# Performance work log

Measured on AMD Instinct MI355X. Metric: run time of the kernel, lower is better.

Reference implementation:

```python
import jax, jax.numpy as jnp
import numpy as np

N_HEADS = 8  # from init_kwargs


def setup_inputs() -> dict:
    key = jax.random.key(0)
    k1, k2, k3 = jax.random.split(key, 3)
    N, Dv, Dk, H, W = 8, 256, 256, 128, 128
    V = jax.random.normal(k1, (N, Dv, H, W), dtype=jnp.float32)
    K = jax.random.normal(k2, (N, Dk, H, W), dtype=jnp.float32)
    Q = jax.random.normal(k3, (N, Dk, H, W), dtype=jnp.float32)
    return {"V": V, "K": K, "Q": Q, "ksize": 5, "dilation": 3}


def _infusion(V, K, Q, ksize, dilation, n_heads):
    # Local dilated-window attention, faithful to the torch im2col version
    # (zero padding => padded taps contribute raw score 0, exp(0)=1 in softmax),
    # but computed shift-by-shift so the (C*k*k, L) unfolded tensors are never
    # materialized.
    N, Dv, H, W = V.shape
    Dk = K.shape[1]
    hd = Dk // n_heads
    vhd = Dv // n_heads
    pad = (ksize // 2) * dilation
    Kp = jnp.pad(K, ((0, 0), (0, 0), (pad, pad), (pad, pad)))
    Vp = jnp.pad(V, ((0, 0), (0, 0), (pad, pad), (pad, pad)))
    Qh = Q.reshape(N, n_heads, hd, H, W)  # channel-major head split, as torch .view

    # scores for each of the ksize*ksize dilated taps: (N, nh, H, W) each
    scores = []
    for fi in range(ksize):
        for fj in range(ksize):
            Ks = Kp[:, :, fi * dilation:fi * dilation + H,
                    fj * dilation:fj * dilation + W].reshape(N, n_heads, hd, H, W)
            scores.append(jnp.einsum('nhdxy,nhdxy->nhxy', Ks, Qh))
    # (N, nh, P, H, W), softmax over window taps P (no 1/sqrt(d) scaling, as in torch)
    att = jax.nn.softmax(jnp.stack(scores, axis=2), axis=2)

    out = jnp.zeros((N, n_heads, vhd, H, W), dtype=V.dtype)
    p = 0
    for fi in range(ksize):
        for fj in range(ksize):
            Vs = Vp[:, :, fi * dilation:fi * dilation + H,
                    fj * dilation:fj * dilation + W].reshape(N, n_heads, vhd, H, W)
            out = out + Vs * att[:, :, p][:, :, None]
            p += 1
    return out.reshape(N, Dv, H, W)


def reference(V, K, Q, ksize, dilation):
    return _infusion(V, K, Q, int(ksize), int(dilation), N_HEADS)
```

## Files before the change

### kernel.cpp

```cpp
#include <hip/hip_runtime.h>


#define Hh 128
#define Ww 128
#define HD 32
#define TAPS 25
#define LROWS 20
#define LSTR 142
#define CHW (LROWS * LSTR)
#define BUFW (2 * CHW)

__global__ __launch_bounds__(256, 2) void infusion_kernel(
    const float* __restrict__ Vt,
    const float* __restrict__ Kt,
    const float* __restrict__ Qt,
    float* __restrict__ Ot)
{
    __shared__ float lbuf[2][BUFW];

    const int tid = threadIdx.x;
    const int tx  = tid & 31;
    const int ty  = tid >> 5;
    const int Rb  = blockIdx.x * 8;
    const int row = Rb + ty;
    const int nh  = blockIdx.y;
    const int xs  = tx << 2;

    const size_t plane = (size_t)Hh * Ww;
    const size_t cbase = (size_t)nh * HD * plane;
    const int qoff = row * Ww + xs;

    bool sgv[3]; int sgo[3]; int sgl[3];
#pragma unroll
    for (int k = 0; k < 3; ++k) {
        const int q  = tid + (k << 8);
        const int lr = q >> 5, xc = q & 31;
        const int r  = Rb + lr - 6;
        const bool ok = (q < 640) && (r >= 0) && (r < Hh);
        sgv[k] = ok;
        sgo[k] = ok ? (r * Ww + (xc << 2)) : 0;
        sgl[k] = (lr < LROWS ? lr : 0) * LSTR + 8 + (xc << 2);
    }

    for (int i = tid; i < 2 * BUFW; i += 256) (&lbuf[0][0])[i] = 0.f;

    float4 stg[6];

    auto loadg = [&](const float* Base, int g) {
        const float* p0 = Base + (size_t)g * plane;
        const float* p1 = p0 + plane;
        stg[0] = *(const float4*)(p0 + sgo[0]);
        stg[1] = *(const float4*)(p0 + sgo[1]);
        stg[2] = *(const float4*)(p0 + sgo[2]);
        stg[3] = *(const float4*)(p1 + sgo[0]);
        stg[4] = *(const float4*)(p1 + sgo[1]);
        stg[5] = *(const float4*)(p1 + sgo[2]);
    };
    auto writeg = [&](int bi) {
#pragma unroll
        for (int cc = 0; cc < 2; ++cc)
#pragma unroll
            for (int k = 0; k < 3; ++k)
                if (sgv[k]) {
                    float* p = &lbuf[bi][cc * CHW + sgl[k]];
                    const float4 v = stg[cc * 3 + k];
                    *(float2*)(p)     = make_float2(v.x, v.y);
                    *(float2*)(p + 2) = make_float2(v.z, v.w);
                }
    };

    float s[4][TAPS];
#pragma unroll
    for (int a = 0; a < 4; ++a)
#pragma unroll
        for (int p = 0; p < TAPS; ++p) s[a][p] = 0.f;

    {
        const float* Kb = Kt + cbase;
        const float* Qb = Qt + cbase;
        float4 qc0 = *(const float4*)(Qb + qoff);
        float4 qc1 = *(const float4*)(Qb + plane + qoff);
        float4 qn0 = qc0, qn1 = qc1;
        loadg(Kb, 0);
        __syncthreads();
        writeg(0);
        loadg(Kb, 2);
        __syncthreads();
#pragma unroll 1
        for (int it = 0; it < 16; ++it) {
            if (it < 15) writeg((it + 1) & 1);
            if (it < 14) loadg(Kb, 2 * it + 4);
            if (it < 15) {
                qn0 = *(const float4*)(Qb + (size_t)(2 * it + 2) * plane + qoff);
                qn1 = *(const float4*)(Qb + (size_t)(2 * it + 3) * plane + qoff);
            }
            const float* lb = &lbuf[it & 1][0];
#pragma unroll
            for (int cc = 0; cc < 2; ++cc) {
                const float4 q = cc ? qc1 : qc0;
#pragma unroll
                for (int fy = 0; fy < 5; ++fy) {
                    const float2* vr =
                        (const float2*)(lb + cc * CHW + (ty + 3 * fy) * LSTR + xs + 2);
                    const float2 w0 = vr[0], w1 = vr[1], w2 = vr[2], w3 = vr[3];
                    const float2 w4 = vr[4], w5 = vr[5], w6 = vr[6], w7 = vr[7];
                    const float v[16] = { w0.x, w0.y, w1.x, w1.y,
                                          w2.x, w2.y, w3.x, w3.y,
                                          w4.x, w4.y, w5.x, w5.y,
                                          w6.x, w6.y, w7.x, w7.y };
#pragma unroll
                    for (int fx = 0; fx < 5; ++fx) {
                        const int p = fy * 5 + fx;
                        s[0][p] = fmaf(v[0 + 3 * fx], q.x, s[0][p]);
                        s[1][p] = fmaf(v[1 + 3 * fx], q.y, s[1][p]);
                        s[2][p] = fmaf(v[2 + 3 * fx], q.z, s[2][p]);
                        s[3][p] = fmaf(v[3 + 3 * fx], q.w, s[3][p]);
                    }
                }
            }
            __syncthreads();
            if (it < 15) { qc0 = qn0; qc1 = qn1; }
        }
    }

    const float* Vb = Vt + cbase;
    float*       Ob = Ot + cbase;
    loadg(Vb, 0);

#pragma unroll
    for (int a = 0; a < 4; ++a) {
        float m = s[a][0];
#pragma unroll
        for (int p = 1; p < TAPS; ++p) m = fmaxf(m, s[a][p]);
        float sum = 0.f;
#pragma unroll
        for (int p = 0; p < TAPS; ++p) { float e = __expf(s[a][p] - m); s[a][p] = e; sum += e; }
        const float rs = 1.0f / sum;
#pragma unroll
        for (int p = 0; p < TAPS; ++p) s[a][p] *= rs;
    }

    {
        writeg(0);
        loadg(Vb, 2);
        __syncthreads();
#pragma unroll 1
        for (int it = 0; it < 16; ++it) {
            if (it < 15) writeg((it + 1) & 1);
            if (it < 14) loadg(Vb, 2 * it + 4);
            const float* lb = &lbuf[it & 1][0];
#pragma unroll
            for (int cc = 0; cc < 2; ++cc) {
                float a0 = 0.f, a1 = 0.f, a2 = 0.f, a3 = 0.f;
#pragma unroll
                for (int fy = 0; fy < 5; ++fy) {
                    const float2* vr =
                        (const float2*)(lb + cc * CHW + (ty + 3 * fy) * LSTR + xs + 2);
                    const float2 w0 = vr[0], w1 = vr[1], w2 = vr[2], w3 = vr[3];
                    const float2 w4 = vr[4], w5 = vr[5], w6 = vr[6], w7 = vr[7];
                    const float v[16] = { w0.x, w0.y, w1.x, w1.y,
                                          w2.x, w2.y, w3.x, w3.y,
                                          w4.x, w4.y, w5.x, w5.y,
                                          w6.x, w6.y, w7.x, w7.y };
#pragma unroll
                    for (int fx = 0; fx < 5; ++fx) {
                        const int p = fy * 5 + fx;
                        a0 = fmaf(v[0 + 3 * fx], s[0][p], a0);
                        a1 = fmaf(v[1 + 3 * fx], s[1][p], a1);
                        a2 = fmaf(v[2 + 3 * fx], s[2][p], a2);
                        a3 = fmaf(v[3 + 3 * fx], s[3][p], a3);
                    }
                }
                *(float4*)(Ob + (size_t)(2 * it + cc) * plane + qoff) =
                    make_float4(a0, a1, a2, a3);
            }
            __syncthreads();
        }
    }
}

extern "C" void kernel_launch(void* const* d_in, const int* in_sizes, int n_in,
                              void* d_out, int out_size, void* d_ws, size_t ws_size,
                              hipStream_t stream) {
    const float* V = (const float*)d_in[0];
    const float* K = (const float*)d_in[1];
    const float* Q = (const float*)d_in[2];
    float* O = (float*)d_out;

    const int N = in_sizes[0] / (256 * Hh * Ww);
    dim3 grid(Hh / 8, N * 8);
    dim3 block(256);
    infusion_kernel<<<grid, block, 0, stream>>>(V, K, Q, O);
}
```

Before: 442.0 us.

## Remap threads to 2 pixels each over 4-row tiles to cut registers

Each thread now computes 2 adjacent pixels instead of 4, and a block covers 4 output rows instead of 8. This halves the per-thread score arrays (50 instead of 100 floats) to ease register pressure. The cost is a larger halo fraction: 16 staged rows for 4 output rows, so K and V are loaded from global memory more times per output. Other changes: shared-memory staging now uses aligned float4 stores, and the trailing barrier after the final iteration is dropped.

Measured after the change: 674.9 us. 1.53x slower.

```diff
diff --git a/kernel.cpp b/kernel.cpp
--- a/kernel.cpp
+++ b/kernel.cpp
@@ -5,10 +5,14 @@
 #define Ww 128
 #define HD 32
 #define TAPS 25
-#define LROWS 20
-#define LSTR 142
+#define TROWS 4
+#define LROWS 16
+#define LSTR 144
 #define CHW (LROWS * LSTR)
-#define BUFW (2 * CHW)
+#define PERW (2 * CHW)
+
+typedef float4 f4;
+typedef float2 f2;
 
 __global__ __launch_bounds__(256, 2) void infusion_kernel(
     const float* __restrict__ Vt,
@@ -16,72 +20,65 @@
     const float* __restrict__ Qt,
     float* __restrict__ Ot)
 {
-    __shared__ float lbuf[2][BUFW];
+    __shared__ alignas(16) float lbuf[2][PERW];
 
     const int tid = threadIdx.x;
-    const int tx  = tid & 31;
-    const int ty  = tid >> 5;
-    const int Rb  = blockIdx.x * 8;
+    const int tx  = tid & 63;
+    const int ty  = tid >> 6;
+    const int Rb  = blockIdx.x * TROWS;
     const int row = Rb + ty;
     const int nh  = blockIdx.y;
-    const int xs  = tx << 2;
+    const int x0  = tx << 1;
 
     const size_t plane = (size_t)Hh * Ww;
     const size_t cbase = (size_t)nh * HD * plane;
-    const int qoff = row * Ww + xs;
+    const int qoff = row * Ww + x0;
 
-    bool sgv[3]; int sgo[3]; int sgl[3];
+    bool sgv[2]; int sgo[2]; float* wp[2];
 #pragma unroll
-    for (int k = 0; k < 3; ++k) {
+    for (int k = 0; k < 2; ++k) {
         const int q  = tid + (k << 8);
         const int lr = q >> 5, xc = q & 31;
         const int r  = Rb + lr - 6;
-        const bool ok = (q < 640) && (r >= 0) && (r < Hh);
+        const bool ok = (r >= 0) && (r < Hh);
         sgv[k] = ok;
         sgo[k] = ok ? (r * Ww + (xc << 2)) : 0;
-        sgl[k] = (lr < LROWS ? lr : 0) * LSTR + 8 + (xc << 2);
+        wp[k]  = &lbuf[0][0] + lr * LSTR + 8 + (xc << 2);
     }
 
-    for (int i = tid; i < 2 * BUFW; i += 256) (&lbuf[0][0])[i] = 0.f;
+    for (int i = tid; i < 2 * PERW; i += 256) (&lbuf[0][0])[i] = 0.f;
 
-    float4 stg[6];
+    const float* Kb = Kt + cbase;
+    const float* Qb = Qt + cbase;
+    const float* Vb = Vt + cbase;
+    float*       Ob = Ot + cbase;
+    const float* lb0 = &lbuf[0][0] + ty * LSTR + x0 + 2;
 
-    auto loadg = [&](const float* Base, int g) {
-        const float* p0 = Base + (size_t)g * plane;
+    f4 stg[4];
+    auto loadg = [&](const float* B, int c0) {
+        const float* p0 = B + (size_t)c0 * plane;
         const float* p1 = p0 + plane;
-        stg[0] = *(const float4*)(p0 + sgo[0]);
-        stg[1] = *(const float4*)(p0 + sgo[1]);
-        stg[2] = *(const float4*)(p0 + sgo[2]);
-        stg[3] = *(const float4*)(p1 + sgo[0]);
-        stg[4] = *(const float4*)(p1 + sgo[1]);
-        stg[5] = *(const float4*)(p1 + sgo[2]);
+        stg[0] = *(const f4*)(p0 + sgo[0]);
+        stg[1] = *(const f4*)(p0 + sgo[1]);
+        stg[2] = *(const f4*)(p1 + sgo[0]);
+        stg[3] = *(const f4*)(p1 + sgo[1]);
     };
     auto writeg = [&](int bi) {
 #pragma unroll
         for (int cc = 0; cc < 2; ++cc)
 #pragma unroll
-            for (int k = 0; k < 3; ++k)
-                if (sgv[k]) {
-                    float* p = &lbuf[bi][cc * CHW + sgl[k]];
-                    const float4 v = stg[cc * 3 + k];
-                    *(float2*)(p)     = make_float2(v.x, v.y);
-                    *(float2*)(p + 2) = make_float2(v.z, v.w);
-                }
+            for (int k = 0; k < 2; ++k)
+                if (sgv[k]) *(f4*)(wp[k] + bi * PERW + cc * CHW) = stg[cc * 2 + k];
     };
 
-    float s[4][TAPS];
+    float s0[TAPS], s1[TAPS];
 #pragma unroll
-    for (int a = 0; a < 4; ++a)
-#pragma unroll
-        for (int p = 0; p < TAPS; ++p) s[a][p] = 0.f;
+    for (int p = 0; p < TAPS; ++p) { s0[p] = 0.f; s1[p] = 0.f; }
 
     {
-        const float* Kb = Kt + cbase;
-        const float* Qb = Qt + cbase;
-        float4 qc0 = *(const float4*)(Qb + qoff);
-        float4 qc1 = *(const float4*)(Qb + plane + qoff);
-        float4 qn0 = qc0, qn1 = qc1;
         loadg(Kb, 0);
+        f2 qc0 = *(const f2*)(Qb + qoff);
+        f2 qc1 = *(const f2*)(Qb + plane + qoff);
         __syncthreads();
         writeg(0);
         loadg(Kb, 2);
@@ -90,91 +87,88 @@
         for (int it = 0; it < 16; ++it) {
             if (it < 15) writeg((it + 1) & 1);
             if (it < 14) loadg(Kb, 2 * it + 4);
+            f2 qn0, qn1;
             if (it < 15) {
-                qn0 = *(const float4*)(Qb + (size_t)(2 * it + 2) * plane + qoff);
-                qn1 = *(const float4*)(Qb + (size_t)(2 * it + 3) * plane + qoff);
+                qn0 = *(const f2*)(Qb + (size_t)(2 * it + 2) * plane + qoff);
+                qn1 = *(const f2*)(Qb + (size_t)(2 * it + 3) * plane + qoff);
             }
-            const float* lb = &lbuf[it & 1][0];
+            const float* lb = lb0 + (it & 1) * PERW;
 #pragma unroll
             for (int cc = 0; cc < 2; ++cc) {
-                const float4 q = cc ? qc1 : qc0;
+                const f2 q = cc ? qc1 : qc0;
 #pragma unroll
                 for (int fy = 0; fy < 5; ++fy) {
-                    const float2* vr =
-                        (const float2*)(lb + cc * CHW + (ty + 3 * fy) * LSTR + xs + 2);
-                    const float2 w0 = vr[0], w1 = vr[1], w2 = vr[2], w3 = vr[3];
-                    const float2 w4 = vr[4], w5 = vr[5], w6 = vr[6], w7 = vr[7];
-                    const float v[16] = { w0.x, w0.y, w1.x, w1.y,
-                                          w2.x, w2.y, w3.x, w3.y,
-                                          w4.x, w4.y, w5.x, w5.y,
-                                          w6.x, w6.y, w7.x, w7.y };
-#pragma unroll
-                    for (int fx = 0; fx < 5; ++fx) {
-                        const int p = fy * 5 + fx;
-                        s[0][p] = fmaf(v[0 + 3 * fx], q.x, s[0][p]);
-                        s[1][p] = fmaf(v[1 + 3 * fx], q.y, s[1][p]);
-                        s[2][p] = fmaf(v[2 + 3 * fx], q.z, s[2][p]);
-                        s[3][p] = fmaf(v[3 + 3 * fx], q.w, s[3][p]);
-                    }
+                    const f2* rp = (const f2*)(lb + cc * CHW + fy * (3 * LSTR));
+                    const f2 w0 = rp[0], w1 = rp[1], w2 = rp[2], w3 = rp[3];
+                    const f2 w4 = rp[4], w5 = rp[5], w6 = rp[6];
+                    const int p = fy * 5;
+                    s0[p + 0] = fmaf(w0.x, q.x, s0[p + 0]);
+                    s0[p + 1] = fmaf(w1.y, q.x, s0[p + 1]);
+                    s0[p + 2] = fmaf(w3.x, q.x, s0[p + 2]);
+                    s0[p + 3] = fmaf(w4.y, q.x, s0[p + 3]);
+                    s0[p + 4] = fmaf(w6.x, q.x, s0[p + 4]);
+                    s1[p + 0] = fmaf(w0.y, q.y, s1[p + 0]);
+                    s1[p + 1] = fmaf(w2.x, q.y, s1[p + 1]);
+                    s1[p + 2] = fmaf(w3.y, q.y, s1[p + 2]);
+                    s1[p + 3] = fmaf(w5.x, q.y, s1[p + 3]);
+                    s1[p + 4] = fmaf(w6.y, q.y, s1[p + 4]);
                 }
             }
-            __syncthreads();
-            if (it < 15) { qc0 = qn0; qc1 = qn1; }
+            if (it < 15) __syncthreads();
+            qc0 = qn0; qc1 = qn1;
         }
     }
 
-    const float* Vb = Vt + cbase;
-    float*       Ob = Ot + cbase;
     loadg(Vb, 0);
 
+    {
+        float m0 = s0[0], m1 = s1[0];
 #pragma unroll
-    for (int a = 0; a < 4; ++a) {
-        float m = s[a][0];
+        for (int p = 1; p < TAPS; ++p) { m0 = fmaxf(m0, s0[p]); m1 = fmaxf(m1, s1[p]); }
+        float t0 = 0.f, t1 = 0.f;
 #pragma unroll
-        for (int p = 1; p < TAPS; ++p) m = fmaxf(m, s[a][p]);
-        float sum = 0.f;
+        for (int p = 0; p < TAPS; ++p) {
+            float e0 = __expf(s0[p] - m0); s0[p] = e0; t0 += e0;
+            float e1 = __expf(s1[p] - m1); s1[p] = e1; t1 += e1;
+        }
+        const float r0 = 1.0f / t0, r1 = 1.0f / t1;
 #pragma unroll
-        for (int p = 0; p < TAPS; ++p) { float e = __expf(s[a][p] - m); s[a][p] = e; sum += e; }
-        const float rs = 1.0f / sum;
-#pragma unroll
-        for (int p = 0; p < TAPS; ++p) s[a][p] *= rs;
+        for (int p = 0; p < TAPS; ++p) { s0[p] *= r0; s1[p] *= r1; }
     }
 
     {
         writeg(0);
         loadg(Vb, 2);
         __syncthreads();
+        float* op = Ob + qoff;
 #pragma unroll 1
         for (int it = 0; it < 16; ++it) {
             if (it < 15) writeg((it + 1) & 1);
             if (it < 14) loadg(Vb, 2 * it + 4);
-            const float* lb = &lbuf[it & 1][0];
+            const float* lb = lb0 + (it & 1) * PERW;
 #pragma unroll
             for (int cc = 0; cc < 2; ++cc) {
-                float a0 = 0.f, a1 = 0.f, a2 = 0.f, a3 = 0.f;
+                float a0 = 0.f, a1 = 0.f;
 #pragma unroll
                 for (int fy = 0; fy < 5; ++fy) {
-                    const float2* vr =
-                        (const float2*)(lb + cc * CHW + (ty + 3 * fy) * LSTR + xs + 2);
-                    const float2 w0 = vr[0], w1 = vr[1], w2 = vr[2], w3 = vr[3];
-                    const float2 w4 = vr[4], w5 = vr[5], w6 = vr[6], w7 = vr[7];
-                    const float v[16] = { w0.x, w0.y, w1.x, w1.y,
-                                          w2.x, w2.y, w3.x, w3.y,
-                                          w4.x, w4.y, w5.x, w5.y,
-                                          w6.x, w6.y, w7.x, w7.y };
-#pragma unroll
-                    for (int fx = 0; fx < 5; ++fx) {
-                        const int p = fy * 5 + fx;
-                        a0 = fmaf(v[0 + 3 * fx], s[0][p], a0);
-                        a1 = fmaf(v[1 + 3 * fx], s[1][p], a1);
-                        a2 = fmaf(v[2 + 3 * fx], s[2][p], a2);
-                        a3 = fmaf(v[3 + 3 * fx], s[3][p], a3);
-                    }
+                    const f2* rp = (const f2*)(lb + cc * CHW + fy * (3 * LSTR));
+                    const f2 w0 = rp[0], w1 = rp[1], w2 = rp[2], w3 = rp[3];
+                    const f2 w4 = rp[4], w5 = rp[5], w6 = rp[6];
+                    const int p = fy * 5;
+                    a0 = fmaf(w0.x, s0[p + 0], a0);
+                    a0 = fmaf(w1.y, s0[p + 1], a0);
+                    a0 = fmaf(w3.x, s0[p + 2], a0);
+                    a0 = fmaf(w4.y, s0[p + 3], a0);
+                    a0 = fmaf(w6.x, s0[p + 4], a0);
+                    a1 = fmaf(w0.y, s1[p + 0], a1);
+                    a1 = fmaf(w2.x, s1[p + 1], a1);
+                    a1 = fmaf(w3.y, s1[p + 2], a1);
+                    a1 = fmaf(w5.x, s1[p + 3], a1);
+                    a1 = fmaf(w6.y, s1[p + 4], a1);
                 }
-                *(float4*)(Ob + (size_t)(2 * it + cc) * plane + qoff) =
-                    make_float4(a0, a1, a2, a3);
+                *(f2*)(op + (size_t)(2 * it + cc) * plane) = make_float2(a0, a1);
             }
-            __syncthreads();
+            if (it < 15) __syncthreads();
         }
     }
 }
@@ -188,7 +182,7 @@
     float* O = (float*)d_out;
 
     const int N = in_sizes[0] / (256 * Hh * Ww);
-    dim3 grid(Hh / 8, N * 8);
+    dim3 grid(Hh / TROWS, N * 8);
     dim3 block(256);
     infusion_kernel<<<grid, block, 0, stream>>>(V, K, Q, O);
 }
```
